# Optimization experiments

Hardware: AMD Instinct MI355X
Metric: run time of the kernel (lower is better)

## Reference

```python
import jax, jax.numpy as jnp
import numpy as np

G = 32        # grid points per axis (in_p is a regular [0,1]^3 grid)
M = 8         # half n_modes (n_modes=16 -> keep 8 low + 8 high per dim, 8 in rfft dim)
NL = 4        # fno_n_layers
HID = 64      # fno_hidden_channels
LIFT = 256    # fno_lifting_channels
NOUT = 16384  # number of output query points
RADIUS = 0.033


def setup_inputs() -> dict:
    key = jax.random.key(0)
    ks = jax.random.split(key, 16)
    g = jnp.linspace(0.0, 1.0, G)
    X, Y, Z = jnp.meshgrid(g, g, g, indexing='ij')
    in_p = jnp.stack([X, Y, Z], -1).astype(jnp.float32)            # [G,G,G,3]
    f = jax.random.normal(ks[0], (G, G, G, 3), jnp.float32)        # [G,G,G,3]
    out_p = jax.random.uniform(ks[1], (NOUT, 3), dtype=jnp.float32)

    def lin(k, i, o):
        return jax.random.normal(k, (i, o), jnp.float32) * (float(i) ** -0.5)

    inp = {
        'in_p': in_p, 'out_p': out_p, 'f': f,
        # Lifting MLP: (in_channels+3)=6 -> 256 -> 64
        'lift_w1': lin(ks[2], 6, LIFT), 'lift_b1': jnp.zeros((LIFT,), jnp.float32),
        'lift_w2': lin(ks[3], LIFT, HID), 'lift_b2': jnp.zeros((HID,), jnp.float32),
        # Spectral weights: [layer, corner(4), in, out, M, M, M, (re,im)]
        'spec_w': jax.random.normal(ks[4], (NL, 4, HID, HID, M, M, M, 2), jnp.float32) * 0.02,
        # Linear (soft) skip per layer
        'skip_w': jax.random.normal(ks[5], (NL, HID, HID), jnp.float32) * (float(HID) ** -0.5),
        'skip_b': jnp.zeros((NL, HID), jnp.float32),
        # GNO kernel MLP: 6 -> 512 -> 256 -> 64
        'gno_w1': lin(ks[6], 6, 512), 'gno_b1': jnp.zeros((512,), jnp.float32),
        'gno_w2': lin(ks[7], 512, 256), 'gno_b2': jnp.zeros((256,), jnp.float32),
        'gno_w3': lin(ks[8], 256, HID), 'gno_b3': jnp.zeros((HID,), jnp.float32),
        # Projection: 64 -> 256 -> 1
        'proj_w1': lin(ks[9], HID, 256), 'proj_b1': jnp.zeros((256,), jnp.float32),
        'proj_w2': lin(ks[10], 256, 1), 'proj_b2': jnp.zeros((1,), jnp.float32),
    }
    return inp


def reference(in_p, out_p, f, lift_w1, lift_b1, lift_w2, lift_b2, spec_w,
              skip_w, skip_b, gno_w1, gno_b1, gno_w2, gno_b2, gno_w3, gno_b3,
              proj_w1, proj_b1, proj_w2, proj_b2):
    gelu = lambda x: jax.nn.gelu(x, approximate=False)

    # ---- FNO latent embedding (channels-last) ----
    h = jnp.concatenate([f, in_p], -1)                               # [G,G,G,6]
    h = gelu(h @ lift_w1 + lift_b1) @ lift_w2 + lift_b2              # [G,G,G,HID]

    w = spec_w[..., 0] + 1j * spec_w[..., 1]                         # [NL,4,i,o,M,M,M]
    lo, hi = slice(0, M), slice(-M, None)
    corners = [(lo, lo), (lo, hi), (hi, lo), (hi, hi)]
    sz = slice(0, M)
    for l in range(NL):
        ft = jnp.fft.rfftn(h, axes=(0, 1, 2), norm='forward')        # [G,G,G//2+1,HID]
        out_ft = jnp.zeros_like(ft)
        for c, (sx, sy) in enumerate(corners):
            blk = jnp.einsum('xyzi,ioxyz->xyzo', ft[sx, sy, sz], w[l, c])
            out_ft = out_ft.at[sx, sy, sz].set(blk)
        hs = jnp.fft.irfftn(out_ft, s=(G, G, G), axes=(0, 1, 2), norm='forward')
        h = hs + h @ skip_w[l] + skip_b[l]
        if l < NL - 1:
            h = gelu(h)
    latent = h.reshape(-1, HID)                                      # [G^3, HID]

    # ---- GNO: radius neighbor search on regular grid + gather-MLP-mean ----
    hgrid = 1.0 / (G - 1)
    i0 = jnp.round(out_p * (G - 1)).astype(jnp.int32)                # nearest cell [N,3]
    off = jnp.stack(jnp.meshgrid(*([jnp.arange(-1, 2)] * 3), indexing='ij'), -1).reshape(-1, 3)
    cand = i0[:, None, :] + off[None]                                # [N,27,3]
    inb = jnp.all((cand >= 0) & (cand < G), -1)
    cc = jnp.clip(cand, 0, G - 1)
    flat = (cc[..., 0] * G + cc[..., 1]) * G + cc[..., 2]            # [N,27]
    ycoord = cc.astype(jnp.float32) * hgrid                          # neighbor coords
    d2 = jnp.sum((out_p[:, None, :] - ycoord) ** 2, -1)
    mask = inb & (d2 <= RADIUS * RADIUS)

    # kernel input = cat([y_coords, x_coords]) per edge -> MLP -> k(x,y) [N,27,HID]
    agg = jnp.concatenate([ycoord, jnp.broadcast_to(out_p[:, None, :], ycoord.shape)], -1)
    k = gelu(agg @ gno_w1 + gno_b1)
    k = gelu(k @ gno_w2 + gno_b2)
    k = k @ gno_w3 + gno_b3
    fy = latent[flat]                                                # gather [N,27,HID]
    msk = mask[..., None].astype(k.dtype)
    num = jnp.sum(k * fy * msk, axis=1)
    den = jnp.maximum(jnp.sum(msk, axis=1), 1.0)
    out = num / den                                                  # [N,HID] (mean reduce)

    # ---- Projection ----
    out = gelu(out @ proj_w1 + proj_b1) @ proj_w2 + proj_b2          # [N,1]
    return out
```

## Files before the change

### kernel.cpp

```cpp
#include <hip/hip_runtime.h>
#include <math.h>


#define ECAP 131072

typedef _Float16 f16x8 __attribute__((ext_vector_type(8)));
typedef float f32x4 __attribute__((ext_vector_type(4)));

__device__ __forceinline__ float gelu_f(float x) {
    float t = fabsf(x) * 0.7071067811865475f;
    float k = __builtin_amdgcn_rcpf(1.0f + 0.3275911f * t);
    float e = __expf(-t * t);
    float y = k*(0.254829592f + k*(-0.284496736f + k*(1.421413741f +
              k*(-1.453152027f + k*1.061405429f))));
    float erfv = 1.0f - y * e;
    return 0.5f * x * (1.0f + copysignf(erfv, x));
}

__global__ __launch_bounds__(256) void k_prep(const float* __restrict__ w2,
                                              const float* __restrict__ w3,
                                              const float* __restrict__ w1,
                                              const float* __restrict__ b1,
                                              const float* __restrict__ lw2,
                                              const float* __restrict__ skw,
                                              const float* __restrict__ out_p,
                                              _Float16* __restrict__ w2T,
                                              _Float16* __restrict__ w3T,
                                              _Float16* __restrict__ w1p,
                                              _Float16* __restrict__ l2hi,
                                              _Float16* __restrict__ l2lo,
                                              _Float16* __restrict__ skwH,
                                              _Float16* __restrict__ skwL,
                                              int* __restrict__ counter,
                                              int* __restrict__ baseG,
                                              int* __restrict__ cntG,
                                              int* __restrict__ eFlat,
                                              float* __restrict__ eAgg)
{
    if (blockIdx.x >= 720) {
        int n = (blockIdx.x - 720)*256 + threadIdx.x;
        const float hg = 1.0f/31.0f;
        const float r2 = (float)(0.033*0.033);
        float px = out_p[n*3+0], py = out_p[n*3+1], pz = out_p[n*3+2];
        int ix = (int)rintf(px*31.f), iy = (int)rintf(py*31.f), iz = (int)rintf(pz*31.f);
        unsigned msk = 0; int cnt = 0;
        for (int j = 0; j < 27; ++j) {
            int dx = j/9 - 1, dy = (j/3)%3 - 1, dz = j%3 - 1;
            int cx = ix+dx, cy = iy+dy, cz = iz+dz;
            bool inb = (cx>=0)&&(cx<32)&&(cy>=0)&&(cy<32)&&(cz>=0)&&(cz<32);
            int qx = min(max(cx,0),31), qy = min(max(cy,0),31), qz = min(max(cz,0),31);
            float yx = qx*hg, yy = qy*hg, yz = qz*hg;
            float d2 = (px-yx)*(px-yx) + (py-yy)*(py-yy) + (pz-yz)*(pz-yz);
            if (inb && d2 <= r2) { msk |= 1u<<j; cnt++; }
        }
        int base = atomicAdd(counter, cnt);
        baseG[n] = base; cntG[n] = cnt;
        int k = 0;
        for (int j = 0; j < 27; ++j) if (msk & (1u<<j)) {
            int dx = j/9 - 1, dy = (j/3)%3 - 1, dz = j%3 - 1;
            int cx = ix+dx, cy = iy+dy, cz = iz+dz;
            int e = base + k;
            eFlat[e] = (cx*32 + cy)*32 + cz;
            eAgg[e*6+0] = cx*hg; eAgg[e*6+1] = cy*hg; eAgg[e*6+2] = cz*hg;
            eAgg[e*6+3] = px;    eAgg[e*6+4] = py;    eAgg[e*6+5] = pz;
            ++k;
        }
        return;
    }
    int idx = blockIdx.x*256 + threadIdx.x;
    if (idx < 131072) {
        int k = idx >> 8, n = idx & 255;
        w2T[n*512 + k] = (_Float16)w2[idx];
    } else if (idx < 147456) {
        int j = idx - 131072;
        int k = j >> 6, o = j & 63;
        w3T[o*256 + k] = (_Float16)w3[j];
    } else if (idx < 151552) {
        int j = idx - 147456;
        int k = j >> 3, d = j & 7;
        float v = d < 6 ? w1[d*512 + k] : (d == 6 ? b1[k] : 0.0f);
        w1p[k*8 + d] = (_Float16)v;
    } else if (idx < 167936) {
        int j = idx - 151552;
        int o = j >> 8, k = j & 255;
        float v = lw2[k*64 + o];
        _Float16 hi = (_Float16)v;
        l2hi[j] = hi;
        l2lo[j] = (_Float16)(v - (float)hi);
    } else if (idx < 184320) {
        int j = idx - 167936;
        int l = j >> 12, r = j & 4095;
        int co = r >> 6, ci = r & 63;
        float v = skw[l*4096 + ci*64 + co];
        _Float16 hi = (_Float16)v;
        skwH[j] = hi;
        skwL[j] = (_Float16)(v - (float)hi);
    }
}

__global__ __launch_bounds__(256) void k_lift(
    const float* __restrict__ f, const float* __restrict__ in_p,
    const float* __restrict__ w1, const float* __restrict__ b1,
    const _Float16* __restrict__ l2hi,
    const _Float16* __restrict__ l2lo,
    const float* __restrict__ b2,
    float* __restrict__ h)
{
    __shared__ __align__(16) _Float16 h1hi[64*264];
    __shared__ __align__(16) _Float16 h1lo[64*264];
    __shared__ float w1s[6*256];
    __shared__ float b1s[256];
    float* oT = (float*)h1hi;
    int t = threadIdx.x;
    for (int i = t; i < 1536; i += 256) w1s[i] = w1[i];
    b1s[t] = b1[t];
    int p0 = blockIdx.x * 64;
    int pt = t >> 2, jq = t & 3;
    int p = p0 + pt;
    float x0 = f[p*3+0], x1 = f[p*3+1], x2 = f[p*3+2];
    float x3 = in_p[p*3+0], x4 = in_p[p*3+1], x5 = in_p[p*3+2];
    __syncthreads();
    for (int r = 0; r < 8; ++r) {
        int j0 = jq*64 + r*8;
        f16x8 vh, vl;
        #pragma unroll
        for (int jj = 0; jj < 8; ++jj) {
            int j = j0 + jj;
            float a = b1s[j] + x0*w1s[j] + x1*w1s[256+j] + x2*w1s[512+j]
                    + x3*w1s[768+j] + x4*w1s[1024+j] + x5*w1s[1280+j];
            float g = gelu_f(a);
            _Float16 hi = (_Float16)g;
            vh[jj] = hi;
            vl[jj] = (_Float16)(g - (float)hi);
        }
        *(f16x8*)&h1hi[pt*264 + j0] = vh;
        *(f16x8*)&h1lo[pt*264 + j0] = vl;
    }
    __syncthreads();
    int w = t >> 6, lane = t & 63, l15 = lane & 15, g = lane >> 4;
    f32x4 acc[4];
    #pragma unroll
    for (int nt = 0; nt < 4; ++nt) {
        float bb = b2[nt*16 + l15];
        acc[nt] = (f32x4){bb, bb, bb, bb};
    }
    for (int kk = 0; kk < 8; ++kk) {
        f16x8 ah = *(const f16x8*)&h1hi[(w*16+l15)*264 + kk*32 + g*8];
        f16x8 al = *(const f16x8*)&h1lo[(w*16+l15)*264 + kk*32 + g*8];
        #pragma unroll
        for (int nt = 0; nt < 4; ++nt) {
            f16x8 bh = *(const f16x8*)&l2hi[(nt*16+l15)*256 + kk*32 + g*8];
            f16x8 bl = *(const f16x8*)&l2lo[(nt*16+l15)*256 + kk*32 + g*8];
            acc[nt] = __builtin_amdgcn_mfma_f32_16x16x32_f16(al, bh, acc[nt], 0, 0, 0);
            acc[nt] = __builtin_amdgcn_mfma_f32_16x16x32_f16(ah, bl, acc[nt], 0, 0, 0);
            acc[nt] = __builtin_amdgcn_mfma_f32_16x16x32_f16(ah, bh, acc[nt], 0, 0, 0);
        }
    }
    __syncthreads();
    #pragma unroll
    for (int nt = 0; nt < 4; ++nt)
        #pragma unroll
        for (int r = 0; r < 4; ++r)
            oT[(nt*16 + l15)*68 + w*16 + g*4 + r] = acc[nt][r];
    __syncthreads();
    for (int i = t; i < 4096; i += 256) {
        int c = i >> 6, ptl = i & 63;
        h[(size_t)c*32768 + p0 + ptl] = oT[c*68 + ptl];
    }
}

__global__ __launch_bounds__(256) void k_fwd_zy(const float* __restrict__ h,
                                                float2* __restrict__ F1)
{
    __shared__ float pl[8*1056];
    __shared__ float2 fz[32*73];
    __shared__ float twc[32], tws[32];
    int t = threadIdx.x;
    int x = blockIdx.x >> 3, cg = blockIdx.x & 7;
    for (int i = t; i < 8192; i += 256) {
        int c = i >> 10, yz = i & 1023;
        pl[c*1056 + (yz>>5)*33 + (yz&31)] = h[(cg*8 + c)*32768 + x*1024 + yz];
    }
    if (t < 32) { float th = (float)t*(6.283185307179586f/32.f); twc[t]=cosf(th); tws[t]=sinf(th); }
    __syncthreads();
    {
        int c = t >> 5, y = t & 31;
        float zv[32];
        #pragma unroll
        for (int z = 0; z < 32; ++z) zv[z] = pl[c*1056 + y*33 + z];
        const float inv = 1.0f/32768.0f;
        #pragma unroll
        for (int kz = 0; kz < 8; ++kz) {
            float re = 0.f, im = 0.f;
            #pragma unroll
            for (int z = 0; z < 32; ++z) {
                int ph = (kz*z)&31;
                re += zv[z]*twc[ph];
                im -= zv[z]*tws[ph];
            }
            fz[y*73 + kz*9 + c] = make_float2(re*inv, im*inv);
        }
    }
    __syncthreads();
    #pragma unroll
    for (int ko = 0; ko < 4; ++ko) {
        int idx = ko*256 + t;
        int kyi = idx >> 6, kz = (idx >> 3) & 7, c = idx & 7;
        int ky = kyi < 8 ? kyi : kyi + 16;
        float re = 0.f, im = 0.f;
        for (int y = 0; y < 32; ++y) {
            int ph = (ky*y)&31;
            float cc = twc[ph], ss = tws[ph];
            float2 a = fz[y*73 + kz*9 + c];
            re += a.x*cc + a.y*ss;
            im += a.y*cc - a.x*ss;
        }
        F1[((kyi*8 + kz)*32 + x)*64 + cg*8 + c] = make_float2(re, im);
    }
}

__global__ __launch_bounds__(256) void k_fwd_x(const float2* __restrict__ F1,
                                               float2* __restrict__ Ft)
{
    __shared__ float2 fs[32*33];
    __shared__ float twc[32], tws[32];
    int t = threadIdx.x;
    int b = blockIdx.x;
    int kyi = b >> 4, kz = (b >> 1) & 7, ih = b & 1;
    const float2* src = &F1[(size_t)((kyi*8 + kz)*32)*64 + ih*32];
    for (int i = t; i < 1024; i += 256) {
        int xx = i >> 5, il = i & 31;
        fs[xx*33 + il] = src[xx*64 + il];
    }
    if (t < 32) { float th = (float)t*(6.283185307179586f/32.f); twc[t]=cosf(th); tws[t]=sinf(th); }
    __syncthreads();
    #pragma unroll
    for (int ko = 0; ko < 2; ++ko) {
        int idx = ko*256 + t;
        int kxi = idx >> 5, il = idx & 31;
        int kx = kxi < 8 ? kxi : kxi + 16;
        float re = 0.f, im = 0.f;
        for (int xx = 0; xx < 32; ++xx) {
            int ph = (kx*xx)&31;
            float cc = twc[ph], ss = tws[ph];
            float2 a = fs[xx*33 + il];
            re += a.x*cc + a.y*ss;
            im += a.y*cc - a.x*ss;
        }
        Ft[((kxi*16 + kyi)*8 + kz)*64 + ih*32 + il] = make_float2(re, im);
    }
}

__global__ __launch_bounds__(256) void k_spec_skip(const float2* __restrict__ Ft,
                                                   const float* __restrict__ spw,
                                                   const float* __restrict__ hold,
                                                   const _Float16* __restrict__ skwH,
                                                   const _Float16* __restrict__ skwL,
                                                   float2* __restrict__ Gt,
                                                   float* __restrict__ hsk,
                                                   int l)
{
    __shared__ __align__(16) char pool[36864];
    int t = threadIdx.x;
    if (blockIdx.x >= 256) {
        _Float16* shi = (_Float16*)pool;
        _Float16* slo = (_Float16*)(pool + 18432);
        int pt0 = (blockIdx.x - 256) * 128;
        for (int i = t; i < 2048; i += 256) {
            int ci = i >> 5, q = i & 31;
            float4 v = *(const float4*)&hold[(size_t)ci*32768 + pt0 + q*4];
            #pragma unroll
            for (int j = 0; j < 4; ++j) {
                float fv = (&v.x)[j];
                _Float16 hi = (_Float16)fv;
                shi[(q*4+j)*72 + ci] = hi;
                slo[(q*4+j)*72 + ci] = (_Float16)(fv - (float)hi);
            }
        }
        __syncthreads();
        int w = t >> 6, lane = t & 63, l15 = lane & 15, g = lane >> 4;
        f32x4 acc[8];
        #pragma unroll
        for (int nt = 0; nt < 8; ++nt) acc[nt] = (f32x4){0.f, 0.f, 0.f, 0.f};
        #pragma unroll
        for (int kk = 0; kk < 2; ++kk) {
            f16x8 ah = *(const f16x8*)&skwH[l*4096 + (w*16+l15)*64 + kk*32 + g*8];
            f16x8 al = *(const f16x8*)&skwL[l*4096 + (w*16+l15)*64 + kk*32 + g*8];
            #pragma unroll
            for (int nt = 0; nt < 8; ++nt) {
                f16x8 bh = *(const f16x8*)&shi[(nt*16+l15)*72 + kk*32 + g*8];
                f16x8 bl = *(const f16x8*)&slo[(nt*16+l15)*72 + kk*32 + g*8];
                acc[nt] = __builtin_amdgcn_mfma_f32_16x16x32_f16(al, bh, acc[nt], 0, 0, 0);
                acc[nt] = __builtin_amdgcn_mfma_f32_16x16x32_f16(ah, bl, acc[nt], 0, 0, 0);
                acc[nt] = __builtin_amdgcn_mfma_f32_16x16x32_f16(ah, bh, acc[nt], 0, 0, 0);
            }
        }
        #pragma unroll
        for (int nt = 0; nt < 8; ++nt)
            #pragma unroll
            for (int r = 0; r < 4; ++r)
                hsk[(size_t)(w*16 + g*4 + r)*32768 + pt0 + nt*16 + l15] = acc[nt][r];
        return;
    }
    float2* ft2 = (float2*)pool;
    int og8 = blockIdx.x >> 5, corner = (blockIdx.x >> 3) & 3, mx = blockIdx.x & 7;
    int kxi = mx + (corner >> 1)*8;
    int kyB = (corner & 1)*8;
    {
        int m = t >> 2, iq = t & 3;
        int my = m >> 3, mz = m & 7;
        int rho = (m >> 1) + ((m & 1) << 5);
        const float2* src = &Ft[(size_t)((kxi*16 + kyB + my)*8 + mz)*64];
        #pragma unroll
        for (int ii = 0; ii < 16; ++ii) {
            int i = iq*16 + ii;
            ft2[rho*65 + i] = src[i];
        }
    }
    __syncthreads();
    int mp = t & 31, oq = t >> 5;
    int o = og8*8 + oq;
    int m0 = 2*mp;
    size_t wbase = (size_t)(l*4 + corner)*4194304 + (size_t)o*1024
                 + (size_t)mx*128 + m0*2;
    float ar0 = 0.f, ai0 = 0.f, ar1 = 0.f, ai1 = 0.f;
    for (int i8 = 0; i8 < 64; i8 += 8) {
        float4 wv[8];
        #pragma unroll
        for (int u = 0; u < 8; ++u)
            wv[u] = *(const float4*)&spw[wbase + (size_t)(i8+u)*65536];
        #pragma unroll
        for (int u = 0; u < 8; ++u) {
            float2 f0 = ft2[mp*65 + i8 + u];
            float2 f1 = ft2[(32 + mp)*65 + i8 + u];
            ar0 += f0.x*wv[u].x - f0.y*wv[u].y;
            ai0 += f0.x*wv[u].y + f0.y*wv[u].x;
            ar1 += f1.x*wv[u].z - f1.y*wv[u].w;
            ai1 += f1.x*wv[u].w + f1.y*wv[u].z;
        }
    }
    size_t gbase = (size_t)(o >> 2)*8192 + (size_t)(corner*8 + mx)*256 + (o & 3);
    Gt[gbase + (size_t)m0*4]       = make_float2(ar0, ai0);
    Gt[gbase + (size_t)(m0+1)*4]   = make_float2(ar1, ai1);
}

__global__ __launch_bounds__(512) void k_inv_zy(const float2* __restrict__ Gt,
                                                const float* __restrict__ hsk,
                                                const float* __restrict__ skb,
                                                float* __restrict__ hnew,
                                                float* __restrict__ latent,
                                                float2* __restrict__ F1,
                                                int l, int do_zy)
{
    __shared__ __align__(16) char pool[58368];
    __shared__ float twc[32], tws[32];
    float2* s1 = (float2*)pool;
    float2* s2 = (float2*)(pool + 8192);
    float*  pl = (float*)(pool + 24576);
    float2* fz = (float2*)pool;

    int t = threadIdx.x;
    int x = blockIdx.x >> 3, cg = blockIdx.x & 7;
    if (t < 32) { float th = (float)t*(6.283185307179586f/32.f); twc[t]=cosf(th); tws[t]=sinf(th); }
    __syncthreads();
    #pragma unroll
    for (int ko = 0; ko < 2; ++ko) {
        int idx = ko*512 + t;
        int kyi = idx >> 6, kz = (idx >> 3) & 7, o = idx & 7;
        int cy = kyi >> 3, my = kyi & 7;
        const float2* gb = Gt + (size_t)(cg*2 + (o>>2))*8192 + my*32 + kz*4 + (o&3);
        float re = 0.f, im = 0.f;
        #pragma unroll
        for (int cxh = 0; cxh < 2; ++cxh) {
            int corner = cxh*2 + cy;
            #pragma unroll
            for (int mxx = 0; mxx < 8; ++mxx) {
                int kxi = cxh*8 + mxx;
                int kx = kxi < 8 ? kxi : kxi + 16;
                int ph = (kx * x) & 31;
                float cc = twc[ph], ss = tws[ph];
                float2 a = gb[(corner*8 + mxx)*256];
                re += a.x*cc - a.y*ss;
                im += a.x*ss + a.y*cc;
            }
        }
        s1[idx] = make_float2(re, im);
    }
    __syncthreads();
    #pragma unroll
    for (int ko = 0; ko < 4; ++ko) {
        int idx = ko*512 + t;
        int y = idx >> 6, kz = (idx >> 3) & 7, o = idx & 7;
        float re = 0.f, im = 0.f;
        #pragma unroll
        for (int kyi = 0; kyi < 16; ++kyi) {
            int ky = kyi < 8 ? kyi : kyi + 16;
            int ph = (ky*y) & 31;
            float cc = twc[ph], ss = tws[ph];
            float2 a = s1[kyi*64 + kz*8 + o];
            re += a.x*cc - a.y*ss;
            im += a.x*ss + a.y*cc;
        }
        s2[idx] = make_float2(re, im);
    }
    __syncthreads();
    {
        float outv[2][8];
        #pragma unroll
        for (int o = 0; o < 8; ++o) {
            float bb = skb[l*64 + cg*8 + o];
            float2 hv = *(const float2*)&hsk[(size_t)(cg*8+o)*32768 + x*1024 + t*2];
            outv[0][o] = bb + hv.x;
            outv[1][o] = bb + hv.y;
        }
        #pragma unroll
        for (int pp = 0; pp < 2; ++pp) {
            int pt = t*2 + pp;
            int y = pt >> 5, z = pt & 31;
            #pragma unroll
            for (int o = 0; o < 8; ++o) {
                float s = s2[y*64 + o].x;
                #pragma unroll
                for (int kz = 1; kz < 8; ++kz) {
                    int ph = (kz*z) & 31;
                    float2 a = s2[y*64 + kz*8 + o];
                    s += 2.0f*(a.x*twc[ph] - a.y*tws[ph]);
                }
                float v = s + outv[pp][o];
                outv[pp][o] = (l < 3) ? gelu_f(v) : v;
            }
        }
        if (l < 3) {
            #pragma unroll
            for (int o = 0; o < 8; ++o) {
                int pt = t*2;
                int y = pt >> 5, z = pt & 31;
                pl[o*1056 + y*33 + z]     = outv[0][o];
                pl[o*1056 + y*33 + z + 1] = outv[1][o];
                *(float2*)&hnew[(size_t)(cg*8+o)*32768 + x*1024 + pt] =
                    make_float2(outv[0][o], outv[1][o]);
            }
        } else {
            #pragma unroll
            for (int pp = 0; pp < 2; ++pp) {
                int pt = t*2 + pp;
                float4 w0 = make_float4(outv[pp][0], outv[pp][1], outv[pp][2], outv[pp][3]);
                float4 w1 = make_float4(outv[pp][4], outv[pp][5], outv[pp][6], outv[pp][7]);
                *(float4*)&latent[(size_t)(x*1024 + pt)*64 + cg*8]     = w0;
                *(float4*)&latent[(size_t)(x*1024 + pt)*64 + cg*8 + 4] = w1;
            }
        }
    }
    if (!do_zy) return;
    __syncthreads();
    {
        int c = t >> 6, y = t & 31, sub = (t >> 5) & 1;
        float zv[32];
        #pragma unroll
        for (int z = 0; z < 32; ++z) zv[z] = pl[c*1056 + y*33 + z];
        const float inv = 1.0f/32768.0f;
        #pragma unroll
        for (int kq = 0; kq < 4; ++kq) {
            int kz = sub*4 + kq;
            float re = 0.f, im = 0.f;
            #pragma unroll
            for (int z = 0; z < 32; ++z) {
                int ph = (kz*z)&31;
                re += zv[z]*twc[ph];
                im -= zv[z]*tws[ph];
            }
            fz[y*73 + kz*9 + c] = make_float2(re*inv, im*inv);
        }
    }
    __syncthreads();
    #pragma unroll
    for (int ko = 0; ko < 2; ++ko) {
        int idx = ko*512 + t;
        int kyi = idx >> 6, kz = (idx >> 3) & 7, c = idx & 7;
        int ky = kyi < 8 ? kyi : kyi + 16;
        float re = 0.f, im = 0.f;
        for (int y = 0; y < 32; ++y) {
            int ph = (ky*y)&31;
            float cc = twc[ph], ss = tws[ph];
            float2 a = fz[y*73 + kz*9 + c];
            re += a.x*cc + a.y*ss;
            im += a.y*cc - a.x*ss;
        }
        F1[((kyi*8 + kz)*32 + x)*64 + cg*8 + c] = make_float2(re, im);
    }
}

__global__ __launch_bounds__(256, 2) void k_gno_mlp(
    const int* __restrict__ counter,
    const int* __restrict__ eFlat,
    const float* __restrict__ eAgg,
    const _Float16* __restrict__ w1p,
    const _Float16* __restrict__ w2T,
    const float* __restrict__ b2,
    const _Float16* __restrict__ w3T,
    const float* __restrict__ b3,
    const float* __restrict__ latent,
    float* __restrict__ kv)
{
    __shared__ __align__(16) _Float16 h1pool[64*520];
    __shared__ __align__(16) _Float16 w1s[512*8];
    __shared__ float aggs[64][6];
    __shared__ int   flatS[64];
    _Float16* h2h = h1pool;

    int t = threadIdx.x;
    int E = counter[0]; if (E > ECAP) E = ECAP;
    int s = blockIdx.x * 64;
    if (s >= E) return;
    int ne = min(64, E - s);

    for (int i = t; i < 512; i += 256)
        ((int4*)w1s)[i] = ((const int4*)w1p)[i];
    for (int i = t; i < 384; i += 256)
        aggs[i/6][i - (i/6)*6] = (i < ne*6) ? eAgg[(size_t)s*6 + i] : 0.0f;
    if (t < 64) flatS[t] = (t < ne) ? eFlat[s + t] : 0;
    __syncthreads();

    int e = t & 63;
    int w = t >> 6;
    {
        float a0 = aggs[e][0], a1 = aggs[e][1], a2 = aggs[e][2];
        float a3 = aggs[e][3], a4 = aggs[e][4], a5 = aggs[e][5];
        int xk = (e >> 3) & 7;
        #pragma unroll
        for (int ci = 0; ci < 16; ++ci) {
            int c = w*16 + ci;
            f16x8 v;
            #pragma unroll
            for (int jj = 0; jj < 8; ++jj) {
                int k = c*8 + jj;
                f16x8 wv = *(const f16x8*)&w1s[k*8];
                float pre = (float)wv[6]
                    + a0*(float)wv[0] + a1*(float)wv[1] + a2*(float)wv[2]
                    + a3*(float)wv[3] + a4*(float)wv[4] + a5*(float)wv[5];
                v[jj] = (_Float16)gelu_f(pre);
            }
            *(f16x8*)&h1pool[e*520 + ((c ^ xk)*8)] = v;
        }
    }
    __syncthreads();

    int lane = t & 63;
    int l15 = lane & 15, g = lane >> 4;

    f32x4 acc2[4][4];
    #pragma unroll
    for (int nt = 0; nt < 4; ++nt) {
        float bb = b2[w*64 + nt*16 + l15];
        #pragma unroll
        for (int mt = 0; mt < 4; ++mt) acc2[mt][nt] = (f32x4){bb, bb, bb, bb};
    }
    #pragma unroll 4
    for (int kk = 0; kk < 16; ++kk) {
        f16x8 af[4];
        #pragma unroll
        for (int mt = 0; mt < 4; ++mt) {
            int ee = mt*16 + l15;
            af[mt] = *(const f16x8*)&h1pool[ee*520 + (((kk*4 + g) ^ ((ee>>3)&7))*8)];
        }
        #pragma unroll
        for (int nt = 0; nt < 4; ++nt) {
            f16x8 bf = *(const f16x8*)&w2T[(size_t)(w*64 + nt*16 + l15)*512 + kk*32 + g*8];
            #pragma unroll
            for (int mt = 0; mt < 4; ++mt)
                acc2[mt][nt] = __builtin_amdgcn_mfma_f32_16x16x32_f16(af[mt], bf, acc2[mt][nt], 0, 0, 0);
        }
    }
    __syncthreads();
    #pragma unroll
    for (int mt = 0; mt < 4; ++mt)
      #pragma unroll
      for (int nt = 0; nt < 4; ++nt) {
        int n = w*64 + nt*16 + l15;
        #pragma unroll
        for (int r = 0; r < 4; ++r) {
            int m = mt*16 + g*4 + r;
            h2h[m*264 + (((n>>3) ^ (m&7))*8) + (n&7)] = (_Float16)gelu_f(acc2[mt][nt][r]);
        }
      }
    __syncthreads();

    int o = w*16 + l15;
    f32x4 acc3[4];
    { float bb = b3[o];
      #pragma unroll
      for (int mt = 0; mt < 4; ++mt) acc3[mt] = (f32x4){bb, bb, bb, bb}; }
    #pragma unroll 2
    for (int kk2 = 0; kk2 < 8; ++kk2) {
        f16x8 bf = *(const f16x8*)&w3T[(size_t)o*256 + kk2*32 + g*8];
        #pragma unroll
        for (int mt = 0; mt < 4; ++mt) {
            int ee = mt*16 + l15;
            f16x8 af = *(const f16x8*)&h2h[ee*264 + (((kk2*4 + g) ^ (ee&7))*8)];
            acc3[mt] = __builtin_amdgcn_mfma_f32_16x16x32_f16(af, bf, acc3[mt], 0, 0, 0);
        }
    }

    #pragma unroll
    for (int mt = 0; mt < 4; ++mt) {
        #pragma unroll
        for (int r = 0; r < 4; ++r) {
            int ee = mt*16 + g*4 + r;
            if (ee < ne) {
                float fy = latent[(size_t)flatS[ee]*64 + o];
                kv[(size_t)(s + ee)*64 + o] = acc3[mt][r] * fy;
            }
        }
    }
}

__global__ __launch_bounds__(256) void k_project(const int* __restrict__ baseG,
                                                 const int* __restrict__ cntG,
                                                 const float* __restrict__ kv,
                                                 const float* __restrict__ pw1,
                                                 const float* __restrict__ pb1,
                                                 const float* __restrict__ pw2,
                                                 const float* __restrict__ pb2,
                                                 float* __restrict__ outp)
{
    __shared__ float w1s[64*260];
    __shared__ float xT[64*68];
    __shared__ float w2s[256];
    __shared__ float b1s[256];
    __shared__ float red[64*4];
    int t = threadIdx.x;
    int p0 = blockIdx.x * 64;
    for (int i = t; i < 16384; i += 256) {
        int k = i >> 8, o = i & 255;
        w1s[k*260 + o] = pw1[i];
    }
    w2s[t] = pw2[t];
    b1s[t] = pb1[t];
    for (int i = t; i < 4096; i += 256) {
        int ptl = i >> 6, c = i & 63;
        int p = p0 + ptl;
        int base = baseG[p], cnt = cntG[p];
        float acc = 0.f;
        for (int j = 0; j < cnt; ++j) acc += kv[(size_t)(base + j)*64 + c];
        xT[c*68 + ptl] = acc / fmaxf((float)cnt, 1.0f);
    }
    __syncthreads();
    int pr = t & 15, oc0 = t >> 4;
    float psum[4] = {0.f, 0.f, 0.f, 0.f};
    for (int it = 0; it < 4; ++it) {
        int oc = it*16 + oc0;
        float a[4][4];
        #pragma unroll
        for (int pp = 0; pp < 4; ++pp)
            #pragma unroll
            for (int q = 0; q < 4; ++q) a[pp][q] = b1s[oc*4 + q];
        for (int i = 0; i < 64; ++i) {
            float4 xv = *(const float4*)&xT[i*68 + pr*4];
            float4 wv = *(const float4*)&w1s[i*260 + oc*4];
            #pragma unroll
            for (int q = 0; q < 4; ++q) {
                float wq = (&wv.x)[q];
                a[0][q] += xv.x*wq; a[1][q] += xv.y*wq;
                a[2][q] += xv.z*wq; a[3][q] += xv.w*wq;
            }
        }
        #pragma unroll
        for (int pp = 0; pp < 4; ++pp) {
            float s = 0.f;
            #pragma unroll
            for (int q = 0; q < 4; ++q) s += gelu_f(a[pp][q]) * w2s[oc*4 + q];
            psum[pp] += s;
        }
    }
    #pragma unroll
    for (int pp = 0; pp < 4; ++pp) {
        psum[pp] += __shfl_xor(psum[pp], 16, 64);
        psum[pp] += __shfl_xor(psum[pp], 32, 64);
    }
    int lane = t & 63, w = t >> 6;
    if (lane < 16) {
        #pragma unroll
        for (int pp = 0; pp < 4; ++pp) red[(lane*4 + pp)*4 + w] = psum[pp];
    }
    __syncthreads();
    if (t < 64)
        outp[p0 + t] = red[t*4+0] + red[t*4+1] + red[t*4+2] + red[t*4+3] + pb2[0];
}

extern "C" void kernel_launch(void* const* d_in, const int* in_sizes, int n_in,
                              void* d_out, int out_size, void* d_ws, size_t ws_size,
                              hipStream_t stream)
{
    const float* in_p = (const float*)d_in[0];
    const float* outp = (const float*)d_in[1];
    const float* f    = (const float*)d_in[2];
    const float* lw1  = (const float*)d_in[3];
    const float* lb1  = (const float*)d_in[4];
    const float* lw2  = (const float*)d_in[5];
    const float* lb2  = (const float*)d_in[6];
    const float* spw  = (const float*)d_in[7];
    const float* skw  = (const float*)d_in[8];
    const float* skb  = (const float*)d_in[9];
    const float* gw1  = (const float*)d_in[10];
    const float* gb1  = (const float*)d_in[11];
    const float* gw2  = (const float*)d_in[12];
    const float* gb2  = (const float*)d_in[13];
    const float* gw3  = (const float*)d_in[14];
    const float* gb3  = (const float*)d_in[15];
    const float* pw1  = (const float*)d_in[16];
    const float* pb1  = (const float*)d_in[17];
    const float* pw2  = (const float*)d_in[18];
    const float* pb2  = (const float*)d_in[19];

    float* ws   = (float*)d_ws;
    float* buf0 = ws;
    float* buf1 = ws + 2097152;
    float* SC   = ws + 4194304;
    float2* F1 = (float2*)SC;
    float2* Ft = (float2*)(SC + 524288);
    float2* Gt = (float2*)(SC + 786432);
    _Float16* w2T  = (_Float16*)(SC + 1048576);
    _Float16* w3T  = (_Float16*)(SC + 1114112);
    _Float16* w1p  = (_Float16*)(SC + 1122304);
    _Float16* l2hi = (_Float16*)(SC + 1124352);
    _Float16* l2lo = (_Float16*)(SC + 1132544);
    _Float16* skwH = (_Float16*)(SC + 1140736);
    _Float16* skwL = (_Float16*)(SC + 1148928);
    int*   counter = (int*)(SC + 1157120);
    int*   baseG   = (int*)(SC + 1157136);
    int*   cntG    = (int*)(SC + 1173520);
    int*   eFlat   = (int*)(SC + 1189904);
    float* eAgg    = SC + 1320976;
    float* kv      = SC + 2107408;
    float* hsk     = SC + 10496016;

    hipMemsetAsync(counter, 0, sizeof(int), stream);
    k_prep<<<784, 256, 0, stream>>>(gw2, gw3, gw1, gb1, lw2, skw, outp,
                                    w2T, w3T, w1p, l2hi, l2lo, skwH, skwL,
                                    counter, baseG, cntG, eFlat, eAgg);
    k_lift<<<512, 256, 0, stream>>>(f, in_p, lw1, lb1, l2hi, l2lo, lb2, buf0);

    k_fwd_zy<<<256, 256, 0, stream>>>(buf0, F1);
    for (int l = 0; l < 4; ++l) {
        const float* hin = (l & 1) ? buf1 : buf0;
        float* hout = (l & 1) ? buf0 : buf1;
        k_fwd_x<<<256, 256, 0, stream>>>(F1, Ft);
        k_spec_skip<<<512, 256, 0, stream>>>(Ft, spw, hin, skwH, skwL, Gt, hsk, l);
        k_inv_zy<<<256, 512, 0, stream>>>(Gt, hsk, skb, hout, buf0, F1,
                                          l, (l < 3) ? 1 : 0);
    }

    k_gno_mlp<<<ECAP/64, 256, 0, stream>>>(counter, eFlat, eAgg,
                                           w1p, w2T, gb2, w3T, gb3, buf0, kv);
    k_project<<<256, 256, 0, stream>>>(baseG, cntG, kv, pw1, pb1, pw2, pb2,
                                       (float*)d_out);
}
```

Baseline: 357.7 us.

## Fuse x-axis forward DFT into spectral multiply kernel, removing k_fwd_x

Removes the separate x-direction forward DFT kernel and its intermediate Ft buffer, computing the needed kx slice directly inside each spectral-multiply block from F1. This saves one launch per layer and a global round trip. The cost is that each block recomputes a DFT over 32 x positions for 64 modes and channels, duplicated across the 32 output-channel groups, greatly increasing L2 reads and ALU work in the spectral blocks.

```diff
diff --git a/kernel.cpp b/kernel.cpp
--- a/kernel.cpp
+++ b/kernel.cpp
@@ -219,39 +219,7 @@
     }
 }
 
-__global__ __launch_bounds__(256) void k_fwd_x(const float2* __restrict__ F1,
-                                               float2* __restrict__ Ft)
-{
-    __shared__ float2 fs[32*33];
-    __shared__ float twc[32], tws[32];
-    int t = threadIdx.x;
-    int b = blockIdx.x;
-    int kyi = b >> 4, kz = (b >> 1) & 7, ih = b & 1;
-    const float2* src = &F1[(size_t)((kyi*8 + kz)*32)*64 + ih*32];
-    for (int i = t; i < 1024; i += 256) {
-        int xx = i >> 5, il = i & 31;
-        fs[xx*33 + il] = src[xx*64 + il];
-    }
-    if (t < 32) { float th = (float)t*(6.283185307179586f/32.f); twc[t]=cosf(th); tws[t]=sinf(th); }
-    __syncthreads();
-    #pragma unroll
-    for (int ko = 0; ko < 2; ++ko) {
-        int idx = ko*256 + t;
-        int kxi = idx >> 5, il = idx & 31;
-        int kx = kxi < 8 ? kxi : kxi + 16;
-        float re = 0.f, im = 0.f;
-        for (int xx = 0; xx < 32; ++xx) {
-            int ph = (kx*xx)&31;
-            float cc = twc[ph], ss = tws[ph];
-            float2 a = fs[xx*33 + il];
-            re += a.x*cc + a.y*ss;
-            im += a.y*cc - a.x*ss;
-        }
-        Ft[((kxi*16 + kyi)*8 + kz)*64 + ih*32 + il] = make_float2(re, im);
-    }
-}
-
-__global__ __launch_bounds__(256) void k_spec_skip(const float2* __restrict__ Ft,
+__global__ __launch_bounds__(256) void k_spec_skip(const float2* __restrict__ F1,
                                                    const float* __restrict__ spw,
                                                    const float* __restrict__ hold,
                                                    const _Float16* __restrict__ skwH,
@@ -261,6 +229,7 @@
                                                    int l)
 {
     __shared__ __align__(16) char pool[36864];
+    __shared__ float twc[32], tws[32];
     int t = threadIdx.x;
     if (blockIdx.x >= 256) {
         _Float16* shi = (_Float16*)pool;
@@ -306,15 +275,31 @@
     int og8 = blockIdx.x >> 5, corner = (blockIdx.x >> 3) & 3, mx = blockIdx.x & 7;
     int kxi = mx + (corner >> 1)*8;
     int kyB = (corner & 1)*8;
+    if (t < 32) { float th = (float)t*(6.283185307179586f/32.f); twc[t]=cosf(th); tws[t]=sinf(th); }
+    __syncthreads();
     {
-        int m = t >> 2, iq = t & 3;
-        int my = m >> 3, mz = m & 7;
-        int rho = (m >> 1) + ((m & 1) << 5);
-        const float2* src = &Ft[(size_t)((kxi*16 + kyB + my)*8 + mz)*64];
-        #pragma unroll
-        for (int ii = 0; ii < 16; ++ii) {
-            int i = iq*16 + ii;
-            ft2[rho*65 + i] = src[i];
+        int w = t >> 6, lane = t & 63;
+        int kx = kxi < 8 ? kxi : kxi + 16;
+        float2 acc[16];
+        #pragma unroll
+        for (int mm = 0; mm < 16; ++mm) acc[mm] = make_float2(0.f, 0.f);
+        for (int x = 0; x < 32; ++x) {
+            int ph = (kx*x) & 31;
+            float cc = twc[ph], ss = tws[ph];
+            #pragma unroll
+            for (int mm = 0; mm < 16; ++mm) {
+                int m = w*16 + mm;
+                int my = m >> 3, mz = m & 7;
+                float2 a = F1[(size_t)((((kyB + my)*8 + mz)*32 + x))*64 + lane];
+                acc[mm].x += a.x*cc + a.y*ss;
+                acc[mm].y += a.y*cc - a.x*ss;
+            }
+        }
+        #pragma unroll
+        for (int mm = 0; mm < 16; ++mm) {
+            int m = w*16 + mm;
+            int rho = (m >> 1) + ((m & 1) << 5);
+            ft2[rho*65 + lane] = acc[mm];
         }
     }
     __syncthreads();
@@ -717,7 +702,6 @@
     float* buf1 = ws + 2097152;
     float* SC   = ws + 4194304;
     float2* F1 = (float2*)SC;
-    float2* Ft = (float2*)(SC + 524288);
     float2* Gt = (float2*)(SC + 786432);
     _Float16* w2T  = (_Float16*)(SC + 1048576);
     _Float16* w3T  = (_Float16*)(SC + 1114112);
@@ -744,8 +728,7 @@
     for (int l = 0; l < 4; ++l) {
         const float* hin = (l & 1) ? buf1 : buf0;
         float* hout = (l & 1) ? buf0 : buf1;
-        k_fwd_x<<<256, 256, 0, stream>>>(F1, Ft);
-        k_spec_skip<<<512, 256, 0, stream>>>(Ft, spw, hin, skwH, skwL, Gt, hsk, l);
+        k_spec_skip<<<512, 256, 0, stream>>>(F1, spw, hin, skwH, skwL, Gt, hsk, l);
         k_inv_zy<<<256, 512, 0, stream>>>(Gt, hsk, skb, hout, buf0, F1,
                                           l, (l < 3) ? 1 : 0);
     }
```

New measurement: 419.3 us. 17.2% more time.
